# Performance work log

Hardware: AMD Instinct MI355X
Metric: run time of the kernel (lower is better)

## Reference

```python
import jax, jax.numpy as jnp
import numpy as np

NUM_HEADS = 16
HEAD_DIM = 64
HIDDEN = NUM_HEADS * HEAD_DIM  # 1024
B, S = 2, 2048


def setup_inputs() -> dict:
    key = jax.random.key(0)
    ks = jax.random.split(key, 6)
    return {
        "hidden_states": jax.random.normal(ks[0], (B, S, HIDDEN), dtype=jnp.float32),
        "lora_state": jax.random.normal(ks[1], (B, S, 3 * HIDDEN), dtype=jnp.float32) * 0.02,
        "w_attn": jax.random.normal(ks[2], (HIDDEN, 3 * HIDDEN), dtype=jnp.float32) * 0.02,
        "b_attn": jax.random.normal(ks[3], (3 * HIDDEN,), dtype=jnp.float32) * 0.02,
        "w_proj": jax.random.normal(ks[4], (HIDDEN, HIDDEN), dtype=jnp.float32) * 0.02,
        "b_proj": jax.random.normal(ks[5], (HIDDEN,), dtype=jnp.float32) * 0.02,
    }


def reference(hidden_states, lora_state, w_attn, b_attn, w_proj, b_proj):
    b, s, d = hidden_states.shape
    # c_attn (GPT2 Conv1D: x @ W + b) plus LoRA correction added pre-split
    qkv = hidden_states @ w_attn + b_attn + lora_state  # [B,S,3D]
    q, k, v = jnp.split(qkv, 3, axis=-1)

    def split_heads(t):  # [B,S,D] -> [B,H,S,hd]
        return t.reshape(b, s, NUM_HEADS, HEAD_DIM).transpose(0, 2, 1, 3)

    q, k, v = split_heads(q), split_heads(k), split_heads(v)

    # eager attention: full [B,H,S,S] scores (faithful to the original)
    attn_weights = jnp.einsum("bhqd,bhkd->bhqk", q, k)
    attn_weights = attn_weights / jnp.asarray(HEAD_DIM ** 0.5, attn_weights.dtype)
    # causal mask via where with finfo.min, as in the torch code
    causal = jnp.tril(jnp.ones((s, s), dtype=bool))
    mask_value = jnp.finfo(attn_weights.dtype).min
    attn_weights = jnp.where(causal[None, None], attn_weights, mask_value)
    attn_weights = jax.nn.softmax(attn_weights, axis=-1)
    # dropout is identity in eval mode
    attn_output = jnp.einsum("bhqk,bhkd->bhqd", attn_weights, v)

    # merge heads [B,H,S,hd] -> [B,S,D]
    attn_output = attn_output.transpose(0, 2, 1, 3).reshape(b, s, d)
    attn_output = attn_output @ w_proj + b_proj
    return attn_output
```

## Files before the change

### kernel.cpp

```cpp
#include <hip/hip_runtime.h>
#include <hip/hip_bf16.h>
#include <cstdint>
#include <cstddef>

typedef unsigned short u16;
typedef unsigned int u32;
using f32x4  = __attribute__((ext_vector_type(4))) float;
using bf16x8 = __attribute__((ext_vector_type(8))) short;

__device__ __forceinline__ u16 f2bf(float f) {
    u32 u = __builtin_bit_cast(u32, f);
    u32 r = u + 0x7fffu + ((u >> 16) & 1u);
    return (u16)(r >> 16);
}

__device__ __forceinline__ void gload16(const u16* g, u16* l) {
    __builtin_amdgcn_global_load_lds(
        (const __attribute__((address_space(1))) void*)g,
        (__attribute__((address_space(3))) void*)l,
        16, 0, 0);
}

__global__ void k_convert(const float* __restrict__ src, u16* __restrict__ dst, int n4) {
    int i = blockIdx.x * blockDim.x + threadIdx.x;
    int stride = gridDim.x * blockDim.x;
    for (; i < n4; i += stride) {
        float4 v = ((const float4*)src)[i];
        ushort4 o;
        o.x = f2bf(v.x); o.y = f2bf(v.y); o.z = f2bf(v.z); o.w = f2bf(v.w);
        ((ushort4*)dst)[i] = o;
    }
}

__global__ void k_tconv(const float* __restrict__ src, u16* __restrict__ dst, int K, int N) {
    __shared__ float tile[32][33];
    int nb = blockIdx.x * 32, kb = blockIdx.y * 32;
    int tx = threadIdx.x, ty = threadIdx.y;
    #pragma unroll
    for (int j = 0; j < 32; j += 8)
        tile[ty + j][tx] = src[(size_t)(kb + ty + j) * N + nb + tx];
    __syncthreads();
    #pragma unroll
    for (int j = 0; j < 32; j += 8)
        dst[(size_t)(nb + ty + j) * K + kb + tx] = f2bf(tile[tx][ty + j]);
}

__device__ __forceinline__ void gemm128_mainloop(const u16* __restrict__ A,
                                                 const u16* __restrict__ Bt,
                                                 int m0, int n0, f32x4 (&acc)[4][4]) {
    __shared__ __align__(16) u16 As[128][32];
    __shared__ __align__(16) u16 Bs[128][32];
    const int t = threadIdx.x;
    const int lane = t & 63, wave = t >> 6;
    const int wr = wave >> 1, wc = wave & 1;
    const int g = lane >> 4, lr = lane & 15;

    #pragma unroll
    for (int mi = 0; mi < 4; mi++)
        #pragma unroll
        for (int ni = 0; ni < 4; ni++)
            acc[mi][ni] = (f32x4){0.f, 0.f, 0.f, 0.f};

    const int q0 = wave * 128 + lane;
    const int q1 = q0 + 64;
    const int r0 = q0 >> 2, c0 = (q0 & 3) * 8;
    const int r1 = q1 >> 2, c1 = (q1 & 3) * 8;
    u16* ldsA0 = &As[0][0] + wave * 1024;
    u16* ldsA1 = ldsA0 + 512;
    u16* ldsB0 = &Bs[0][0] + wave * 1024;
    u16* ldsB1 = ldsB0 + 512;
    const u16* gA0 = A  + (size_t)(m0 + r0) * 1024 + c0;
    const u16* gA1 = A  + (size_t)(m0 + r1) * 1024 + c1;
    const u16* gB0 = Bt + (size_t)(n0 + r0) * 1024 + c0;
    const u16* gB1 = Bt + (size_t)(n0 + r1) * 1024 + c1;

    for (int kt = 0; kt < 1024; kt += 32) {
        __syncthreads();
        gload16(gA0 + kt, ldsA0);
        gload16(gA1 + kt, ldsA1);
        gload16(gB0 + kt, ldsB0);
        gload16(gB1 + kt, ldsB1);
        __syncthreads();
        bf16x8 af[4], bfr[4];
        #pragma unroll
        for (int mi = 0; mi < 4; mi++)
            af[mi] = *(const bf16x8*)&As[wr * 64 + mi * 16 + lr][g * 8];
        #pragma unroll
        for (int ni = 0; ni < 4; ni++)
            bfr[ni] = *(const bf16x8*)&Bs[wc * 64 + ni * 16 + lr][g * 8];
        #pragma unroll
        for (int mi = 0; mi < 4; mi++)
            #pragma unroll
            for (int ni = 0; ni < 4; ni++)
                acc[mi][ni] = __builtin_amdgcn_mfma_f32_16x16x32_bf16(af[mi], bfr[ni], acc[mi][ni], 0, 0, 0);
    }
}

__global__ __launch_bounds__(256) void k_gemm_qkv(const u16* __restrict__ Xb, const u16* __restrict__ Wab,
                                                  const float* __restrict__ lora, const float* __restrict__ b_attn,
                                                  u16* __restrict__ Qb, u16* __restrict__ Kb, u16* __restrict__ Vt) {
    f32x4 acc[4][4];
    const int m0 = blockIdx.y * 128, n0 = blockIdx.x * 128;
    gemm128_mainloop(Xb, Wab, m0, n0, acc);
    const int lane = threadIdx.x & 63, wave = threadIdx.x >> 6;
    const int wr = wave >> 1, wc = wave & 1, g = lane >> 4, lr = lane & 15;
    #pragma unroll
    for (int mi = 0; mi < 4; mi++)
        #pragma unroll
        for (int ni = 0; ni < 4; ni++)
            #pragma unroll
            for (int r = 0; r < 4; r++) {
                int m = m0 + wr * 64 + mi * 16 + g * 4 + r;
                int n = n0 + wc * 64 + ni * 16 + lr;
                float v = acc[mi][ni][r] + b_attn[n] + lora[(size_t)m * 3072 + n];
                int which = n >> 10, rem = n & 1023, h = rem >> 6, hd = rem & 63;
                int b = m >> 11, s = m & 2047;
                size_t idx = ((size_t)(b * 16 + h) * 2048 + s) * 64 + hd;
                if (which == 0)      Qb[idx] = f2bf(v * 0.125f);
                else if (which == 1) Kb[idx] = f2bf(v);
                else Vt[((size_t)(b * 16 + h) * 64 + hd) * 2048 + s] = f2bf(v);
            }
}

__device__ __forceinline__ void attn_tile(const u16 (*Ks)[72], const u16 (*Vs)[72], u16 (*Ps)[72],
                                          int g, int lr, int rowq , int k0, bool diag,
                                          bf16x8 qf0, bf16x8 qf1,
                                          f32x4 (&accO)[4], float (&m_run)[4], float (&l_run)[4]) {
    f32x4 sc[4];
    #pragma unroll
    for (int ni = 0; ni < 4; ni++) {
        bf16x8 kf0 = *(const bf16x8*)&Ks[ni * 16 + lr][g * 8];
        bf16x8 kf1 = *(const bf16x8*)&Ks[ni * 16 + lr][32 + g * 8];
        f32x4 z = {0.f, 0.f, 0.f, 0.f};
        z = __builtin_amdgcn_mfma_f32_16x16x32_bf16(qf0, kf0, z, 0, 0, 0);
        z = __builtin_amdgcn_mfma_f32_16x16x32_bf16(qf1, kf1, z, 0, 0, 0);
        sc[ni] = z;
    }
    if (diag) {
        #pragma unroll
        for (int ni = 0; ni < 4; ni++)
            #pragma unroll
            for (int r = 0; r < 4; r++)
                if (k0 + ni * 16 + lr > rowq + g * 4 + r) sc[ni][r] = -INFINITY;
    }
    #pragma unroll
    for (int r = 0; r < 4; r++) {
        float mx = fmaxf(fmaxf(sc[0][r], sc[1][r]), fmaxf(sc[2][r], sc[3][r]));
        #pragma unroll
        for (int d = 1; d < 16; d <<= 1) mx = fmaxf(mx, __shfl_xor(mx, d, 64));
        float mnew = fmaxf(m_run[r], mx);
        float fsc = __expf(m_run[r] - mnew);
        float ls = 0.f;
        #pragma unroll
        for (int ni = 0; ni < 4; ni++) {
            float p = __expf(sc[ni][r] - mnew);
            sc[ni][r] = p;
            ls += p;
        }
        #pragma unroll
        for (int d = 1; d < 16; d <<= 1) ls += __shfl_xor(ls, d, 64);
        #pragma unroll
        for (int di = 0; di < 4; di++) accO[di][r] *= fsc;
        m_run[r] = mnew;
        l_run[r] = l_run[r] * fsc + ls;
    }
    #pragma unroll
    for (int ni = 0; ni < 4; ni++)
        #pragma unroll
        for (int r = 0; r < 4; r++)
            Ps[g * 4 + r][ni * 16 + lr] = f2bf(sc[ni][r]);
    #pragma unroll
    for (int e = 0; e < 2; e++) {
        bf16x8 pa = *(const bf16x8*)&Ps[lr][e * 32 + g * 8];
        #pragma unroll
        for (int di = 0; di < 4; di++) {
            bf16x8 vb = *(const bf16x8*)&Vs[di * 16 + lr][e * 32 + g * 8];
            accO[di] = __builtin_amdgcn_mfma_f32_16x16x32_bf16(pa, vb, accO[di], 0, 0, 0);
        }
    }
}

__global__ __launch_bounds__(256) void k_attn(const u16* __restrict__ Qb, const u16* __restrict__ Kb,
                                              const u16* __restrict__ Vt, u16* __restrict__ Ao) {
    __shared__ __align__(16) u16 Ks[64][72];
    __shared__ __align__(16) u16 Vs[64][72];
    __shared__ __align__(16) u16 Ps[4][16][72];
    const int i = blockIdx.x, bh = blockIdx.y;
    const int qtA = i, qtB = 31 - i;
    const int t = threadIdx.x, wave = t >> 6, lane = t & 63;
    const int g = lane >> 4, lr = lane & 15;
    const size_t bhO = (size_t)bh * (2048 * 64);
    const int q0A = qtA * 64, q0B = qtB * 64;
    const int rowqA = q0A + wave * 16, rowqB = q0B + wave * 16;

    bf16x8 qfA0 = *(const bf16x8*)(Qb + bhO + (size_t)(rowqA + lr) * 64 + g * 8);
    bf16x8 qfA1 = *(const bf16x8*)(Qb + bhO + (size_t)(rowqA + lr) * 64 + 32 + g * 8);
    bf16x8 qfB0 = *(const bf16x8*)(Qb + bhO + (size_t)(rowqB + lr) * 64 + g * 8);
    bf16x8 qfB1 = *(const bf16x8*)(Qb + bhO + (size_t)(rowqB + lr) * 64 + 32 + g * 8);

    f32x4 accA[4], accB[4];
    float mA[4], lA[4], mB[4], lB[4];
    #pragma unroll
    for (int x = 0; x < 4; x++) {
        accA[x] = (f32x4){0.f,0.f,0.f,0.f}; accB[x] = (f32x4){0.f,0.f,0.f,0.f};
        mA[x] = -INFINITY; lA[x] = 0.f; mB[x] = -INFINITY; lB[x] = 0.f;
    }

    const int sr0 = t >> 3,         sj0 = t & 7;
    const int sr1 = (t + 256) >> 3, sj1 = (t + 256) & 7;
    const u16* gK0 = Kb + bhO + (size_t)sr0 * 64 + sj0 * 8;
    const u16* gK1 = Kb + bhO + (size_t)sr1 * 64 + sj1 * 8;
    const u16* gV0 = Vt + bhO + (size_t)sr0 * 2048 + sj0 * 8;
    const u16* gV1 = Vt + bhO + (size_t)sr1 * 2048 + sj1 * 8;

    uint4 pk0 = *(const uint4*)(gK0);
    uint4 pk1 = *(const uint4*)(gK1);
    uint4 pv0 = *(const uint4*)(gV0);
    uint4 pv1 = *(const uint4*)(gV1);

    for (int kt = 0; kt <= qtB; ++kt) {
        const int k0 = kt * 64;
        __syncthreads();
        *(uint4*)&Ks[sr0][sj0 * 8] = pk0;
        *(uint4*)&Ks[sr1][sj1 * 8] = pk1;
        *(uint4*)&Vs[sr0][sj0 * 8] = pv0;
        *(uint4*)&Vs[sr1][sj1 * 8] = pv1;
        __syncthreads();

        if (kt < qtB) {
            const size_t kn = (size_t)(k0 + 64);
            pk0 = *(const uint4*)(gK0 + kn * 64);
            pk1 = *(const uint4*)(gK1 + kn * 64);
            pv0 = *(const uint4*)(gV0 + kn);
            pv1 = *(const uint4*)(gV1 + kn);
        }

        if (kt <= qtA)
            attn_tile(Ks, Vs, Ps[wave], g, lr, rowqA, k0, kt == qtA, qfA0, qfA1, accA, mA, lA);
        attn_tile(Ks, Vs, Ps[wave], g, lr, rowqB, k0, kt == qtB, qfB0, qfB1, accB, mB, lB);
    }

    const int b = bh >> 4, h = bh & 15;
    #pragma unroll
    for (int di = 0; di < 4; di++)
        #pragma unroll
        for (int r = 0; r < 4; r++) {
            int sA = rowqA + g * 4 + r;
            int sB = rowqB + g * 4 + r;
            Ao[((size_t)(b * 2048 + sA)) * 1024 + h * 64 + di * 16 + lr] = f2bf(accA[di][r] / lA[r]);
            Ao[((size_t)(b * 2048 + sB)) * 1024 + h * 64 + di * 16 + lr] = f2bf(accB[di][r] / lB[r]);
        }
}

__global__ __launch_bounds__(256) void k_gemm_proj(const u16* __restrict__ Ao, const u16* __restrict__ Wpb,
                                                   const float* __restrict__ b_proj, float* __restrict__ out) {
    f32x4 acc[4][4];
    const int m0 = blockIdx.y * 128, n0 = blockIdx.x * 128;
    gemm128_mainloop(Ao, Wpb, m0, n0, acc);
    const int lane = threadIdx.x & 63, wave = threadIdx.x >> 6;
    const int wr = wave >> 1, wc = wave & 1, g = lane >> 4, lr = lane & 15;
    #pragma unroll
    for (int mi = 0; mi < 4; mi++)
        #pragma unroll
        for (int ni = 0; ni < 4; ni++)
            #pragma unroll
            for (int r = 0; r < 4; r++) {
                int m = m0 + wr * 64 + mi * 16 + g * 4 + r;
                int n = n0 + wc * 64 + ni * 16 + lr;
                out[(size_t)m * 1024 + n] = acc[mi][ni][r] + b_proj[n];
            }
}

extern "C" void kernel_launch(void* const* d_in, const int* in_sizes, int n_in,
                              void* d_out, int out_size, void* d_ws, size_t ws_size,
                              hipStream_t stream) {
    const float* hidden = (const float*)d_in[0];
    const float* lora   = (const float*)d_in[1];
    const float* w_attn = (const float*)d_in[2];
    const float* b_attn = (const float*)d_in[3];
    const float* w_proj = (const float*)d_in[4];
    const float* b_proj = (const float*)d_in[5];
    float* out = (float*)d_out;

    char* ws = (char*)d_ws;
    u16* Xb  = (u16*)(ws + 0x0);
    u16* Wab = (u16*)(ws + 0x800000);
    u16* Wpb = (u16*)(ws + 0xE00000);
    u16* Qb  = (u16*)(ws + 0x1000000);
    u16* Kb  = (u16*)(ws + 0x1800000);
    u16* Vt  = (u16*)(ws + 0x2000000);
    u16* Ao  = Xb;

    k_convert<<<1024, 256, 0, stream>>>(hidden, Xb, (2 * 2048 * 1024) / 4);
    k_tconv<<<dim3(96, 32), dim3(32, 8), 0, stream>>>(w_attn, Wab, 1024, 3072);
    k_tconv<<<dim3(32, 32), dim3(32, 8), 0, stream>>>(w_proj, Wpb, 1024, 1024);
    k_gemm_qkv<<<dim3(24, 32), 256, 0, stream>>>(Xb, Wab, lora, b_attn, Qb, Kb, Vt);
    k_attn<<<dim3(16, 32), 256, 0, stream>>>(Qb, Kb, Vt, Ao);
    k_gemm_proj<<<dim3(8, 32), 256, 0, stream>>>(Ao, Wpb, b_proj, out);
}
```

Before: 318.4 us.

## Double-buffer LDS tiles in GEMM mainloop to overlap loads with MFMA

The 128x128 GEMM mainloop now uses two LDS buffers for the A and B tiles. The global-to-LDS load of the next k-slice is issued before the MFMA compute on the current slice, and a single waitcnt plus barrier replaces the two syncthreads per iteration. This is meant to hide global load latency behind compute. In exchange it doubles LDS use per block, which may reduce occupancy, and it relies on manual waitcnt and barrier correctness.

```diff
diff --git a/kernel.cpp b/kernel.cpp
--- a/kernel.cpp
+++ b/kernel.cpp
@@ -48,8 +48,8 @@
 __device__ __forceinline__ void gemm128_mainloop(const u16* __restrict__ A,
                                                  const u16* __restrict__ Bt,
                                                  int m0, int n0, f32x4 (&acc)[4][4]) {
-    __shared__ __align__(16) u16 As[128][32];
-    __shared__ __align__(16) u16 Bs[128][32];
+    __shared__ __align__(16) u16 As[2][128][32];
+    __shared__ __align__(16) u16 Bs[2][128][32];
     const int t = threadIdx.x;
     const int lane = t & 63, wave = t >> 6;
     const int wr = wave >> 1, wc = wave & 1;
@@ -65,34 +65,49 @@
     const int q1 = q0 + 64;
     const int r0 = q0 >> 2, c0 = (q0 & 3) * 8;
     const int r1 = q1 >> 2, c1 = (q1 & 3) * 8;
-    u16* ldsA0 = &As[0][0] + wave * 1024;
-    u16* ldsA1 = ldsA0 + 512;
-    u16* ldsB0 = &Bs[0][0] + wave * 1024;
-    u16* ldsB1 = ldsB0 + 512;
+    u16* lA0 = &As[0][0][0] + wave * 1024;
+    u16* lA1 = &As[1][0][0] + wave * 1024;
+    u16* lB0 = &Bs[0][0][0] + wave * 1024;
+    u16* lB1 = &Bs[1][0][0] + wave * 1024;
     const u16* gA0 = A  + (size_t)(m0 + r0) * 1024 + c0;
     const u16* gA1 = A  + (size_t)(m0 + r1) * 1024 + c1;
     const u16* gB0 = Bt + (size_t)(n0 + r0) * 1024 + c0;
     const u16* gB1 = Bt + (size_t)(n0 + r1) * 1024 + c1;
 
-    for (int kt = 0; kt < 1024; kt += 32) {
-        __syncthreads();
-        gload16(gA0 + kt, ldsA0);
-        gload16(gA1 + kt, ldsA1);
-        gload16(gB0 + kt, ldsB0);
-        gload16(gB1 + kt, ldsB1);
-        __syncthreads();
+    auto STAGE = [&](u16* la, u16* lb, int kt) {
+        gload16(gA0 + kt, la);
+        gload16(gA1 + kt, la + 512);
+        gload16(gB0 + kt, lb);
+        gload16(gB1 + kt, lb + 512);
+    };
+    auto COMPUTE = [&](const u16 (*Asb)[32], const u16 (*Bsb)[32]) {
         bf16x8 af[4], bfr[4];
         #pragma unroll
         for (int mi = 0; mi < 4; mi++)
-            af[mi] = *(const bf16x8*)&As[wr * 64 + mi * 16 + lr][g * 8];
-        #pragma unroll
-        for (int ni = 0; ni < 4; ni++)
-            bfr[ni] = *(const bf16x8*)&Bs[wc * 64 + ni * 16 + lr][g * 8];
+            af[mi] = *(const bf16x8*)&Asb[wr * 64 + mi * 16 + lr][g * 8];
+        #pragma unroll
+        for (int ni = 0; ni < 4; ni++)
+            bfr[ni] = *(const bf16x8*)&Bsb[wc * 64 + ni * 16 + lr][g * 8];
         #pragma unroll
         for (int mi = 0; mi < 4; mi++)
             #pragma unroll
             for (int ni = 0; ni < 4; ni++)
                 acc[mi][ni] = __builtin_amdgcn_mfma_f32_16x16x32_bf16(af[mi], bfr[ni], acc[mi][ni], 0, 0, 0);
+    };
+
+    STAGE(lA0, lB0, 0);
+    asm volatile("s_waitcnt vmcnt(0)" ::: "memory");
+    __builtin_amdgcn_s_barrier();
+
+    for (int kt = 0; kt < 1024; kt += 64) {
+        if (kt + 32 < 1024) STAGE(lA1, lB1, kt + 32);
+        COMPUTE(As[0], Bs[0]);
+        asm volatile("s_waitcnt vmcnt(0)" ::: "memory");
+        __builtin_amdgcn_s_barrier();
+        if (kt + 64 < 1024) STAGE(lA0, lB0, kt + 64);
+        COMPUTE(As[1], Bs[1]);
+        asm volatile("s_waitcnt vmcnt(0)" ::: "memory");
+        __builtin_amdgcn_s_barrier();
     }
 }
 
```

New measurement: 322.3 us. No clear change (+1.2%).
